# Performance work log

Measured on AMD Instinct MI355X. Metric: run time of the kernel, lower is better.

The kernel has to match this reference:

```python
import jax, jax.numpy as jnp
import numpy as np

B, V = 256, 128000

def setup_inputs() -> dict:
    key = jax.random.key(0)
    k1, k2, k3 = jax.random.split(key, 3)
    logits = jax.random.normal(k1, (B, V), dtype=jnp.float32)
    temperatures = jax.random.uniform(k2, (B,), dtype=jnp.float32)
    top_ps = jax.random.uniform(k3, (B,), dtype=jnp.float32)
    return {"logits": logits, "temperatures": temperatures, "top_ps": top_ps}

def reference(logits, temperatures, top_ps):
    logits = logits.astype(jnp.float32)
    greedy_tokens = jnp.argmax(logits, axis=-1)
    t = temperatures[:, None]
    greedy_mask = t <= 1e-10                       # [B, 1]
    safe_t = jnp.maximum(t, 1e-5)
    probs = jax.nn.softmax(logits / safe_t, axis=-1)  # [B, V]
    # descending sort of probs with indices
    order = jnp.argsort(-probs, axis=-1)           # [B, V]
    sorted_probs = jnp.take_along_axis(probs, order, axis=-1)
    cum = jnp.cumsum(sorted_probs, axis=-1)
    mask = cum > top_ps[:, None]
    mask = mask.at[:, 0].set(False)                # always keep top-1
    sorted_probs = jnp.where(mask, 0.0, sorted_probs)
    # scatter the masked probs back to original vocab positions
    rows = jnp.arange(B)[:, None]
    probs = jnp.zeros_like(probs).at[rows, order].set(sorted_probs)
    probs = probs / jnp.sum(probs, axis=-1, keepdims=True)
    # Gumbel-max style sampling: argmax(probs / Exp(1) noise)
    noise = jax.random.exponential(jax.random.key(1), probs.shape, dtype=jnp.float32)
    noise = jnp.maximum(noise, 1e-10)
    sample_tokens = jnp.argmax(probs / noise, axis=-1)
    return jnp.where(greedy_mask[:, 0], greedy_tokens, sample_tokens)
```

## Files before the change

kernel.cpp:

```cpp
#include <hip/hip_runtime.h>
#include <stdint.h>

typedef unsigned long long u64;
typedef uint32_t u32;

#define BB 256
#define VV 128000
#define NV4 (VV / 4)
#define SLICES 16
#define SL4 (NV4 / SLICES)
#define NBUCK 4096
#define CAP 2048
#define QSCALE 1.099511627776e12f
#define QINV   (1.0 / 1099511627776.0)

#define OFF_SMAX 0
#define OFF_SARG (16*1024)
#define OFF_WWIN (32*1024)
#define OFF_PAR  (64*1024)
#define OFF_CNT  (72*1024)
#define OFF_HIST (80*1024)
#define OFF_LIST (OFF_HIST + (size_t)BB*NBUCK*8)
#define WS_TOTAL (OFF_LIST + (size_t)BB*CAP*8)

struct RowPar { int bstar; float thr; double M; double cutZ; };

#if defined(__has_builtin)
# if __has_builtin(__builtin_amdgcn_sched_barrier)
#  define SCHED_FENCE() __builtin_amdgcn_sched_barrier(0)
# endif
#endif
#ifndef SCHED_FENCE
# define SCHED_FENCE() asm volatile("" ::: "memory")
#endif

__device__ __forceinline__ u32 rotl32(u32 v, u32 r) { return (v << r) | (v >> (32u - r)); }

__device__ __forceinline__ u32 threefry_bits(u32 j) {
    const u32 ks0 = 0u, ks1 = 1u, ks2 = 0x1BD11BDBu;
    u32 x0 = ks0, x1 = j + ks1;
    x0 += x1; x1 = rotl32(x1, 13); x1 ^= x0;
    x0 += x1; x1 = rotl32(x1, 15); x1 ^= x0;
    x0 += x1; x1 = rotl32(x1, 26); x1 ^= x0;
    x0 += x1; x1 = rotl32(x1, 6);  x1 ^= x0;
    x0 += ks1; x1 += ks2 + 1u;
    x0 += x1; x1 = rotl32(x1, 17); x1 ^= x0;
    x0 += x1; x1 = rotl32(x1, 29); x1 ^= x0;
    x0 += x1; x1 = rotl32(x1, 16); x1 ^= x0;
    x0 += x1; x1 = rotl32(x1, 24); x1 ^= x0;
    x0 += ks2; x1 += ks0 + 2u;
    x0 += x1; x1 = rotl32(x1, 13); x1 ^= x0;
    x0 += x1; x1 = rotl32(x1, 15); x1 ^= x0;
    x0 += x1; x1 = rotl32(x1, 26); x1 ^= x0;
    x0 += x1; x1 = rotl32(x1, 6);  x1 ^= x0;
    x0 += ks0; x1 += ks1 + 3u;
    x0 += x1; x1 = rotl32(x1, 17); x1 ^= x0;
    x0 += x1; x1 = rotl32(x1, 29); x1 ^= x0;
    x0 += x1; x1 = rotl32(x1, 16); x1 ^= x0;
    x0 += x1; x1 = rotl32(x1, 24); x1 ^= x0;
    x0 += ks1; x1 += ks2 + 4u;
    x0 += x1; x1 = rotl32(x1, 13); x1 ^= x0;
    x0 += x1; x1 = rotl32(x1, 15); x1 ^= x0;
    x0 += x1; x1 = rotl32(x1, 26); x1 ^= x0;
    x0 += x1; x1 = rotl32(x1, 6);  x1 ^= x0;
    x0 += ks2; x1 += ks0 + 5u;
    return x0 ^ x1;
}

__device__ __forceinline__ float q_of(float x, float invT, float xm) {
    return __expf(fmaf(x, invT, -xm));
}

__device__ __forceinline__ float noise_of(u32 j) {
    u32 bits = threefry_bits(j);
    float u = __uint_as_float((bits >> 9) | 0x3F800000u) - 1.0f;
    return fmaxf(-log1pf(-u), 1e-10f);
}

__device__ __forceinline__ void noise2_of(u32 ja, u32 jb, float& na, float& nb) {
    const u32 ks0 = 0u, ks1 = 1u, ks2 = 0x1BD11BDBu;
    u32 a0 = ks0, a1 = ja + ks1;
    u32 b0 = ks0, b1 = jb + ks1;
#define TF2_RND(r) a0 += a1; a1 = rotl32(a1, r); a1 ^= a0; \
                   b0 += b1; b1 = rotl32(b1, r); b1 ^= b0;
    TF2_RND(13) TF2_RND(15) TF2_RND(26) TF2_RND(6)
    a0 += ks1; a1 += ks2 + 1u;  b0 += ks1; b1 += ks2 + 1u;
    TF2_RND(17) TF2_RND(29) TF2_RND(16) TF2_RND(24)
    a0 += ks2; a1 += ks0 + 2u;  b0 += ks2; b1 += ks0 + 2u;
    TF2_RND(13) TF2_RND(15) TF2_RND(26) TF2_RND(6)
    a0 += ks0; a1 += ks1 + 3u;  b0 += ks0; b1 += ks1 + 3u;
    TF2_RND(17) TF2_RND(29) TF2_RND(16) TF2_RND(24)
    a0 += ks1; a1 += ks2 + 4u;  b0 += ks1; b1 += ks2 + 4u;
    TF2_RND(13) TF2_RND(15) TF2_RND(26) TF2_RND(6)
    a0 += ks2; a1 += ks0 + 5u;  b0 += ks2; b1 += ks0 + 5u;
#undef TF2_RND
    u32 xa = a0 ^ a1, xb = b0 ^ b1;
    float ua = __uint_as_float((xa >> 9) | 0x3F800000u) - 1.0f;
    float ub = __uint_as_float((xb >> 9) | 0x3F800000u) - 1.0f;
    na = fmaxf(-log1pf(-ua), 1e-10f);
    nb = fmaxf(-log1pf(-ub), 1e-10f);
}

extern "C" __global__ void __launch_bounds__(256, 1)
k1_stats(const float* __restrict__ logits, float* __restrict__ smax,
         int* __restrict__ sarg, u64* __restrict__ Whist, int* __restrict__ Wcnt) {
    int blk = blockIdx.x, r = blk >> 4, s = blk & 15;
    int tid = threadIdx.x, lane = tid & 63, wid = tid >> 6;
    __shared__ float sf[4]; __shared__ int si[4];
    Whist[(size_t)r * NBUCK + s * 256 + tid] = 0ULL;
    if (s == 0 && tid == 0) Wcnt[r] = 0;
    const float4* L4 = (const float4*)(logits + (size_t)r * VV);
    int i0 = s * SL4 + tid;
    bool h7 = tid < (SL4 - 7 * 256);
    float4 b0 = L4[i0],          b1 = L4[i0 + 256],  b2 = L4[i0 + 512];
    float4 b3 = L4[i0 + 768],    b4 = L4[i0 + 1024], b5 = L4[i0 + 1280];
    float4 b6 = L4[i0 + 1536],   b7 = L4[h7 ? i0 + 1792 : i0];
    SCHED_FENCE();
    float m = -3.402823466e38f; int mi = 0x7FFFFFFF;
    auto upd = [&](float4 a, int iv) {
        float m4 = fmaxf(fmaxf(a.x, a.y), fmaxf(a.z, a.w));
        if (m4 > m) {
            int base = iv * 4;
            if      (a.x == m4) mi = base;
            else if (a.y == m4) mi = base + 1;
            else if (a.z == m4) mi = base + 2;
            else                mi = base + 3;
            m = m4;
        }
    };
    upd(b0, i0);        upd(b1, i0 + 256);  upd(b2, i0 + 512);  upd(b3, i0 + 768);
    upd(b4, i0 + 1024); upd(b5, i0 + 1280); upd(b6, i0 + 1536);
    if (h7) upd(b7, i0 + 1792);
    for (int off = 32; off; off >>= 1) {
        float ov = __shfl_down(m, off); int oi = __shfl_down(mi, off);
        if (ov > m || (ov == m && oi < mi)) { m = ov; mi = oi; }
    }
    if (lane == 0) { sf[wid] = m; si[wid] = mi; }
    __syncthreads();
    if (tid == 0) {
        for (int w = 1; w < 4; w++) {
            float ov = sf[w]; int oi = si[w];
            if (ov > m || (ov == m && oi < mi)) { m = ov; mi = oi; }
        }
        smax[blk] = m; sarg[blk] = mi;
    }
}

extern "C" __global__ void __launch_bounds__(256, 1)
k2_hist(const float* __restrict__ logits, const float* __restrict__ smax,
        const float* __restrict__ temps, u64* __restrict__ Whist) {
    __shared__ u64 lh[NBUCK];
    int blk = blockIdx.x, r = blk >> 4, s = blk & 15, tid = threadIdx.x;
    for (int i = tid; i < NBUCK; i += 256) lh[i] = 0ULL;
    float T = fmaxf(temps[r], 1e-5f), invT = 1.0f / T;
    float rm = -3.402823466e38f;
    for (int j = 0; j < 16; j++) rm = fmaxf(rm, smax[r * 16 + j]);
    float xm = rm * invT;
    __syncthreads();
    const float4* L4 = (const float4*)(logits + (size_t)r * VV);
    int i0 = s * SL4 + tid;
    bool h7 = tid < (SL4 - 7 * 256);
    float4 b0 = L4[i0],          b1 = L4[i0 + 256],  b2 = L4[i0 + 512];
    float4 b3 = L4[i0 + 768],    b4 = L4[i0 + 1024], b5 = L4[i0 + 1280];
    float4 b6 = L4[i0 + 1536],   b7 = L4[h7 ? i0 + 1792 : i0];
    SCHED_FENCE();
    auto proc = [&](float4 x) {
        float xs[4] = {x.x, x.y, x.z, x.w};
        #pragma unroll
        for (int k = 0; k < 4; k++) {
            float t = fmaf(xs[k], invT, -xm);
            if (t < -27.75f) continue;
            float q = __expf(t);
            u32 pb = __float_as_uint(q);
            if (pb) atomicAdd(&lh[pb >> 18], (u64)(q * QSCALE));
        }
    };
    proc(b0); proc(b1); proc(b2); proc(b3); proc(b4); proc(b5); proc(b6);
    if (h7) proc(b7);
    __syncthreads();
    u64* gh = Whist + (size_t)r * NBUCK;
    for (int i = tid; i < NBUCK; i += 256) {
        u64 v = lh[i];
        if (v) atomicAdd(&gh[i], v);
    }
}

extern "C" __global__ void __launch_bounds__(1024)
k3_cut(const u64* __restrict__ Whist, const float* __restrict__ topps,
       RowPar* __restrict__ par) {
    int r = blockIdx.x, tid = threadIdx.x, lane = tid & 63, wid = tid >> 6;
    __shared__ double wtot[16];
    __shared__ double sh_cutZ; __shared__ int sh_b; __shared__ double sh_M;
    const u64* gh = Whist + (size_t)r * NBUCK;
    double h0 = (double)gh[4 * tid]     * QINV;
    double h1 = (double)gh[4 * tid + 1] * QINV;
    double h2 = (double)gh[4 * tid + 2] * QINV;
    double h3 = (double)gh[4 * tid + 3] * QINV;
    double s3 = h3, s2 = s3 + h2, s1 = s2 + h1, s0 = s1 + h0;
    double incl = s0;
    for (int off = 1; off < 64; off <<= 1) {
        double u = __shfl_down(incl, off);
        if (lane + off < 64) incl += u;
    }
    double excl = __shfl_down(incl, 1); if (lane == 63) excl = 0.0;
    if (lane == 0) wtot[wid] = incl;
    if (tid == 0) { sh_b = -1; sh_M = 0.0; }
    __syncthreads();
    double cw = 0.0;
    for (int w = wid + 1; w < 16; w++) cw += wtot[w];
    double carry = excl + cw;
    if (tid == 0) sh_cutZ = (double)topps[r] * (s0 + carry);
    __syncthreads();
    double cutZ = sh_cutZ;
    double S0 = s0 + carry, S1 = s1 + carry, S2 = s2 + carry, S3 = s3 + carry;
    if (S0 > cutZ && S1 <= cutZ)    { sh_b = 4 * tid;     sh_M = S1; }
    if (S1 > cutZ && S2 <= cutZ)    { sh_b = 4 * tid + 1; sh_M = S2; }
    if (S2 > cutZ && S3 <= cutZ)    { sh_b = 4 * tid + 2; sh_M = S3; }
    if (S3 > cutZ && carry <= cutZ) { sh_b = 4 * tid + 3; sh_M = carry; }
    __syncthreads();
    if (tid == 0) {
        float thr = -3.402823466e38f;
        if (sh_b > 0) {
            float qlo = __uint_as_float((u32)sh_b << 18);
            if (qlo >= 1.17549435e-38f) thr = logf(qlo) - 1e-3f;
        }
        RowPar p; p.bstar = sh_b; p.thr = thr; p.M = sh_M; p.cutZ = cutZ;
        par[r] = p;
    }
}

extern "C" __global__ void __launch_bounds__(256, 1)
k4_race(const float* __restrict__ logits, const float* __restrict__ smax,
        const float* __restrict__ temps, const RowPar* __restrict__ par,
        int* __restrict__ Wcnt, u64* __restrict__ Wlist, u64* __restrict__ Wwin) {
    int blk = blockIdx.x, r = blk >> 4, s = blk & 15;
    int tid = threadIdx.x, lane = tid & 63, wid = tid >> 6;
    __shared__ u64 seg[2][4][257];
    __shared__ int qn[2][4];
    __shared__ u64 wred[4];
    float T = fmaxf(temps[r], 1e-5f), invT = 1.0f / T;
    float rm = -3.402823466e38f;
    for (int j = 0; j < 16; j++) rm = fmaxf(rm, smax[r * 16 + j]);
    float xm = rm * invT;
    int bstar = par[r].bstar;
    float thr = par[r].thr;
    const float4* L4 = (const float4*)(logits + (size_t)r * VV);
    u32 jbase = (u32)r * (u32)VV;
    u64 pk = 0ULL;
    const u64 lanelt = (1ULL << lane) - 1ULL;
    const int dsg = tid & 3, idxb = tid >> 2;
    int i0 = s * SL4 + tid;
    bool h7 = tid < (SL4 - 7 * 256);
    float4 b0 = L4[i0],          b1 = L4[i0 + 256],  b2 = L4[i0 + 512];
    float4 b3 = L4[i0 + 768],    b4 = L4[i0 + 1024], b5 = L4[i0 + 1280];
    float4 b6 = L4[i0 + 1536],   b7 = L4[h7 ? i0 + 1792 : i0];
    SCHED_FENCE();

    auto kfilter = [&](int ph, float4 v, int off, bool valid) {
        float t0 = fmaf(v.x, invT, -xm), t1 = fmaf(v.y, invT, -xm);
        float t2 = fmaf(v.z, invT, -xm), t3 = fmaf(v.w, invT, -xm);
        int base = (i0 + off) * 4;
        bool p0 = valid && (t0 >= thr), p1 = valid && (t1 >= thr);
        bool p2 = valid && (t2 >= thr), p3 = valid && (t3 >= thr);
        u64 m0 = __ballot(p0), m1 = __ballot(p1);
        u64 m2 = __ballot(p2), m3 = __ballot(p3);
        int c0 = __popcll(m0), c01 = c0 + __popcll(m1), c012 = c01 + __popcll(m2);
        u64* sg = seg[ph][wid];
        if (p0) sg[       __popcll(m0 & lanelt)] = ((u64)__float_as_uint(t0) << 32) | (u32)(base + 0);
        if (p1) sg[c0   + __popcll(m1 & lanelt)] = ((u64)__float_as_uint(t1) << 32) | (u32)(base + 1);
        if (p2) sg[c01  + __popcll(m2 & lanelt)] = ((u64)__float_as_uint(t2) << 32) | (u32)(base + 2);
        if (p3) sg[c012 + __popcll(m3 & lanelt)] = ((u64)__float_as_uint(t3) << 32) | (u32)(base + 3);
        if (lane == 0) qn[ph][wid] = c012 + __popcll(m3);
    };

    auto kproc2 = [&](u64 ea, u64 eb, bool va, bool vb) {
        float ta = __uint_as_float((u32)(ea >> 32));
        float tb = __uint_as_float((u32)(eb >> 32));
        u32 dva = (u32)ea, dvb = (u32)eb;
        float qa = __expf(ta), qb = __expf(tb);
        u32 pba = __float_as_uint(qa), pbb = __float_as_uint(qb);
        int bba = (int)(pba >> 18), bbb = (int)(pbb >> 18);
        bool ra = va && pba && (bba > bstar);
        bool rb = vb && pbb && (bbb > bstar);
        if (ra || rb) {
            float nza, nzb;
            noise2_of(jbase + dva, jbase + dvb, nza, nzb);
            if (ra) {
                float sc = __fdividef(qa, nza);
                u64 ee = ((u64)__float_as_uint(sc) << 32) | (u64)(~dva);
                if (ee > pk) pk = ee;
            }
            if (rb) {
                float sc = __fdividef(qb, nzb);
                u64 ee = ((u64)__float_as_uint(sc) << 32) | (u64)(~dvb);
                if (ee > pk) pk = ee;
            }
        }
        if (va && pba && bba == bstar) {
            int pos = atomicAdd(&Wcnt[r], 1);
            if (pos < CAP)
                Wlist[(size_t)r * CAP + pos] = ((u64)pba << 32) | (u64)(~dva);
        }
        if (vb && pbb && bbb == bstar) {
            int pos = atomicAdd(&Wcnt[r], 1);
            if (pos < CAP)
                Wlist[(size_t)r * CAP + pos] = ((u64)pbb << 32) | (u64)(~dvb);
        }
    };
    auto kdense = [&](int ph) {
        int cnt = qn[ph][dsg];
        const u64* sg = seg[ph][dsg];
        u64 e0 = sg[idxb], e1 = sg[idxb + 64], e2 = sg[idxb + 128], e3 = sg[idxb + 192];
        bool v0 = idxb < cnt, v1 = idxb + 64 < cnt;
        bool v2 = idxb + 128 < cnt, v3 = idxb + 192 < cnt;
        if (v0 | v1) kproc2(e0, e1, v0, v1);
        if (v2 | v3) kproc2(e2, e3, v2, v3);
    };

    kfilter(0, b0, 0, true);
    __syncthreads();
    kfilter(1, b1, 256, true);   kdense(0);
    __syncthreads();
    kfilter(0, b2, 512, true);   kdense(1);
    __syncthreads();
    kfilter(1, b3, 768, true);   kdense(0);
    __syncthreads();
    kfilter(0, b4, 1024, true);  kdense(1);
    __syncthreads();
    kfilter(1, b5, 1280, true);  kdense(0);
    __syncthreads();
    kfilter(0, b6, 1536, true);  kdense(1);
    __syncthreads();
    kfilter(1, b7, 1792, h7);    kdense(0);
    __syncthreads();
    kdense(1);

    for (int off = 32; off; off >>= 1) { u64 o = __shfl_down(pk, off); if (o > pk) pk = o; }
    if (lane == 0) wred[wid] = pk;
    __syncthreads();
    if (tid == 0) {
        for (int w = 1; w < 4; w++) if (wred[w] > pk) pk = wred[w];
        Wwin[blk] = pk;
    }
}

extern "C" __global__ void __launch_bounds__(1024)
k5_final(const float* __restrict__ smax, const int* __restrict__ sarg,
         const float* __restrict__ temps, const float* __restrict__ topps,
         const RowPar* __restrict__ par, const int* __restrict__ Wcnt,
         const u64* __restrict__ Wlist, const u64* __restrict__ Wwin,
         int* __restrict__ out) {
    int r = blockIdx.x, tid = threadIdx.x, lane = tid & 63, wid = tid >> 6;
    __shared__ u64 sb[CAP];
    __shared__ double wtot[16];
    __shared__ u64 wred[16];
    __shared__ int sh_js, sh_n, sh_gidx; __shared__ float sh_rm;
    RowPar p = par[r];
    if (tid == 0) {
        float rm = -3.402823466e38f; int gi = 0x7FFFFFFF;
        for (int j = 0; j < 16; j++) {
            float v = smax[r * 16 + j];
            if (v > rm) { rm = v; gi = sarg[r * 16 + j]; }
        }
        sh_rm = rm; sh_gidx = gi;
        int n = Wcnt[r]; if (n > CAP) n = CAP; sh_n = n;
        sh_js = 0x7FFFFFFF;
    }
    __syncthreads();
    int n = sh_n;
    int npad = 4; while (npad < n) npad <<= 1;
    const u64* lst = Wlist + (size_t)r * CAP;
    for (int i = tid; i < npad; i += 1024) sb[i] = (i < n) ? lst[i] : 0ULL;
    __syncthreads();
    for (int k = 2; k <= npad; k <<= 1) {
        for (int j = k >> 1; j > 0; j >>= 1) {
            for (int i = tid; i < npad; i += 1024) {
                int q2 = i ^ j;
                if (q2 > i) {
                    u64 a = sb[i], b = sb[q2];
                    bool desc = ((i & k) == 0);
                    if (desc ? (a < b) : (a > b)) { sb[i] = b; sb[q2] = a; }
                }
            }
            __syncthreads();
        }
    }
    int t2 = tid * 2;
    double f0 = 0.0, f1 = 0.0;
    if (t2 < npad) {
        f0 = (double)__uint_as_float((u32)(sb[t2] >> 32));
        f1 = (double)__uint_as_float((u32)(sb[t2 + 1] >> 32));
    }
    double c0 = f0, c1 = c0 + f1;
    double incl = c1;
    for (int off = 1; off < 64; off <<= 1) {
        double u = __shfl_up(incl, off);
        if (lane >= off) incl += u;
    }
    double excl = __shfl_up(incl, 1); if (lane == 0) excl = 0.0;
    double wt = __shfl(incl, 63);
    if (lane == 0) wtot[wid] = wt;
    __syncthreads();
    double cw = 0.0;
    for (int w = 0; w < wid; w++) cw += wtot[w];
    double cr = cw + excl;
    if (t2 < npad) {
        bool m0 = (p.M + (cr + c0)) > p.cutZ;
        bool m1 = (p.M + (cr + c1)) > p.cutZ;
        int cand = m0 ? t2 : m1 ? (t2 + 1) : 0x7FFFFFFF;
        if (cand != 0x7FFFFFFF) atomicMin(&sh_js, cand);
    }
    __syncthreads();
    float Traw = temps[r];
    if (tid == 0) {
        int js = sh_js; if (js > n) js = n;
        float T = fmaxf(Traw, 1e-5f), invT = 1.0f / T, xm = sh_rm * invT;
        int btop = (int)(__float_as_uint(q_of(sh_rm, invT, xm)) >> 18);
        if (js == 0 && p.bstar == btop) js = 1;
        sh_js = js;
    }
    __syncthreads();
    int js = sh_js;
    u32 jbase = (u32)r * (u32)VV;
    u64 pk = 0ULL;
    for (int i = tid; i < js; i += 1024) {
        u64 key = sb[i];
        float qq = __uint_as_float((u32)(key >> 32));
        u32 v = ~(u32)key;
        float nz = noise_of(jbase + v);
        float sc = __fdividef(qq, nz);
        u64 e = ((u64)__float_as_uint(sc) << 32) | (u64)(~v);
        if (e > pk) pk = e;
    }
    if (tid < 16) { u64 w = Wwin[r * 16 + tid]; if (w > pk) pk = w; }
    for (int off = 32; off; off >>= 1) { u64 o = __shfl_down(pk, off); if (o > pk) pk = o; }
    if (lane == 0) wred[wid] = pk;
    __syncthreads();
    if (tid == 0) {
        for (int w = 1; w < 16; w++) if (wred[w] > pk) pk = wred[w];
        int bi = (int)(~(u32)pk);
        out[r] = (Traw <= 1e-10f) ? sh_gidx : bi;
    }
}

extern "C" __global__ void __launch_bounds__(1024, 1)
sampler_fallback(const float* __restrict__ logits, const float* __restrict__ temps,
                 const float* __restrict__ topps, int* __restrict__ out)
{
    const int row = blockIdx.x;
    const int tid = threadIdx.x;
    const int lane = tid & 63;
    const int wid = tid >> 6;
    const float* L = logits + (size_t)row * VV;
    const float4* L4 = (const float4*)L;
    __shared__ __align__(16) unsigned char SMEM[32768];
    float* hist = (float*)SMEM;
    u64* sortbuf = (u64*)SMEM;
    __shared__ double wtot[16];
    __shared__ float wredf[16];
    __shared__ int wredi[16];
    __shared__ float sh_lmax;
    __shared__ int sh_gidx;
    __shared__ double sh_cutZ;
    __shared__ double sh_M;
    __shared__ int sh_bstar;
    __shared__ int sh_ng;
    __shared__ int sh_jstar;
    const float Traw = temps[row];
    const float T = fmaxf(Traw, 1e-5f);
    const float invT = 1.0f / T;
    const float tp = topps[row];
    float lmax = -3.402823466e38f; int lidx = 0x7FFFFFFF;
    for (int iv = tid; iv < NV4; iv += 1024) {
        float4 x = L4[iv];
        float m4 = fmaxf(fmaxf(x.x, x.y), fmaxf(x.z, x.w));
        if (m4 > lmax) {
            int base = iv * 4;
            if      (x.x == m4) lidx = base;
            else if (x.y == m4) lidx = base + 1;
            else if (x.z == m4) lidx = base + 2;
            else                lidx = base + 3;
            lmax = m4;
        }
    }
    for (int off = 32; off > 0; off >>= 1) {
        float ov = __shfl_down(lmax, off);
        int   oi = __shfl_down(lidx, off);
        if (ov > lmax || (ov == lmax && oi < lidx)) { lmax = ov; lidx = oi; }
    }
    if (lane == 0) { wredf[wid] = lmax; wredi[wid] = lidx; }
    for (int i = tid; i < NBUCK; i += 1024) hist[i] = 0.0f;
    __syncthreads();
    if (wid == 0) {
        float v = (lane < 16) ? wredf[lane] : -3.402823466e38f;
        int   i = (lane < 16) ? wredi[lane] : 0x7FFFFFFF;
        for (int off = 32; off > 0; off >>= 1) {
            float ov = __shfl_down(v, off);
            int   oi = __shfl_down(i, off);
            if (ov > v || (ov == v && oi < i)) { v = ov; i = oi; }
        }
        if (lane == 0) { sh_lmax = v; sh_gidx = i; }
    }
    __syncthreads();
    const float xm = sh_lmax * invT;
    const int gidx = sh_gidx;
    const int btop = (int)(__float_as_uint(q_of(sh_lmax, invT, xm)) >> 18);
    for (int iv = tid; iv < NV4; iv += 1024) {
        float4 x = L4[iv];
        float q0 = q_of(x.x, invT, xm), q1 = q_of(x.y, invT, xm);
        float q2 = q_of(x.z, invT, xm), q3 = q_of(x.w, invT, xm);
        u32 b0 = __float_as_uint(q0), b1 = __float_as_uint(q1);
        u32 b2 = __float_as_uint(q2), b3 = __float_as_uint(q3);
        if (b0) atomicAdd(&hist[b0 >> 18], q0);
        if (b1) atomicAdd(&hist[b1 >> 18], q1);
        if (b2) atomicAdd(&hist[b2 >> 18], q2);
        if (b3) atomicAdd(&hist[b3 >> 18], q3);
    }
    __syncthreads();
    float h0 = hist[4 * tid], h1 = hist[4 * tid + 1],
          h2 = hist[4 * tid + 2], h3 = hist[4 * tid + 3];
    double s3 = (double)h3, s2 = s3 + (double)h2, s1 = s2 + (double)h1, s0 = s1 + (double)h0;
    double incl = s0;
    for (int off = 1; off < 64; off <<= 1) {
        double u = __shfl_down(incl, off);
        if (lane + off < 64) incl += u;
    }
    double excl = __shfl_down(incl, 1);
    if (lane == 63) excl = 0.0;
    if (lane == 0) wtot[wid] = incl;
    __syncthreads();
    double cw = 0.0;
    for (int w = wid + 1; w < 16; w++) cw += wtot[w];
    const double carry = excl + cw;
    if (tid == 0) {
        sh_cutZ = (double)tp * (s0 + carry);
        sh_bstar = -1; sh_M = 0.0; sh_ng = 0; sh_jstar = 0x7FFFFFFF;
    }
    __syncthreads();
    const double cutZ = sh_cutZ;
    {
        double S0 = s0 + carry, S1 = s1 + carry, S2 = s2 + carry, S3 = s3 + carry;
        if (S0 > cutZ && S1 <= cutZ)    { sh_bstar = 4 * tid;     sh_M = S1; }
        if (S1 > cutZ && S2 <= cutZ)    { sh_bstar = 4 * tid + 1; sh_M = S2; }
        if (S2 > cutZ && S3 <= cutZ)    { sh_bstar = 4 * tid + 2; sh_M = S3; }
        if (S3 > cutZ && carry <= cutZ) { sh_bstar = 4 * tid + 3; sh_M = carry; }
    }
    __syncthreads();
    const int bstar = sh_bstar;
    const double M = sh_M;
    float bs = -1.0f; int bi = 0x7FFFFFFF;
    const u32 jbase = (u32)row * (u32)VV;
    for (int iv = tid; iv < NV4; iv += 1024) {
        float4 x = L4[iv];
        float qs[4] = {q_of(x.x, invT, xm), q_of(x.y, invT, xm),
                       q_of(x.z, invT, xm), q_of(x.w, invT, xm)};
        int base = iv * 4;
        #pragma unroll
        for (int k = 0; k < 4; k++) {
            u32 pb = __float_as_uint(qs[k]);
            if (pb == 0u) continue;
            int b = (int)(pb >> 18);
            if (b > bstar) {
                int v = base + k;
                float nz = noise_of(jbase + (u32)v);
                float sc = __fdividef(qs[k], nz);
                if (sc > bs || (sc == bs && v < bi)) { bs = sc; bi = v; }
            } else if (b == bstar) {
                int pos = atomicAdd(&sh_ng, 1);
                if (pos < 4096)
                    sortbuf[pos] = ((u64)pb << 32) | (u32)(~(u32)(base + k));
            }
        }
    }
    __syncthreads();
    if (bstar >= 0) {
        int n = sh_ng; if (n > 4096) n = 4096;
        int npad = 4; while (npad < n) npad <<= 1;
        for (int i = tid; i < npad; i += 1024) if (i >= n) sortbuf[i] = 0ULL;
        __syncthreads();
        for (int k = 2; k <= npad; k <<= 1) {
            for (int j = k >> 1; j > 0; j >>= 1) {
                for (int i = tid; i < npad; i += 1024) {
                    int pidx = i ^ j;
                    if (pidx > i) {
                        u64 a = sortbuf[i], b2 = sortbuf[pidx];
                        bool desc = ((i & k) == 0);
                        if (desc ? (a < b2) : (a > b2)) { sortbuf[i] = b2; sortbuf[pidx] = a; }
                    }
                }
                __syncthreads();
            }
        }
        double f0 = 0.0, f1 = 0.0, f2 = 0.0, f3 = 0.0;
        int t4 = tid * 4;
        if (t4 < npad) {
            f0 = (double)__uint_as_float((u32)(sortbuf[t4]     >> 32));
            f1 = (double)__uint_as_float((u32)(sortbuf[t4 + 1] >> 32));
            f2 = (double)__uint_as_float((u32)(sortbuf[t4 + 2] >> 32));
            f3 = (double)__uint_as_float((u32)(sortbuf[t4 + 3] >> 32));
        }
        double c0 = f0, c1 = c0 + f1, c2 = c1 + f2, c3 = c2 + f3;
        double incl2 = c3;
        for (int off = 1; off < 64; off <<= 1) {
            double u = __shfl_up(incl2, off);
            if (lane >= off) incl2 += u;
        }
        double excl2 = __shfl_up(incl2, 1);
        if (lane == 0) excl2 = 0.0;
        double wt = __shfl(incl2, 63);
        if (lane == 0) wtot[wid] = wt;
        __syncthreads();
        double cw2 = 0.0;
        for (int w = 0; w < wid; w++) cw2 += wtot[w];
        double cr = cw2 + excl2;
        if (t4 < npad) {
            bool m0 = (M + (cr + c0)) > cutZ;
            bool m1 = (M + (cr + c1)) > cutZ;
            bool m2 = (M + (cr + c2)) > cutZ;
            bool m3 = (M + (cr + c3)) > cutZ;
            int cand = m0 ? t4 : m1 ? (t4 + 1) : m2 ? (t4 + 2) : m3 ? (t4 + 3) : 0x7FFFFFFF;
            if (cand != 0x7FFFFFFF) atomicMin(&sh_jstar, cand);
        }
        __syncthreads();
        int jstar = sh_jstar; if (jstar > n) jstar = n;
        if (jstar == 0 && bstar == btop) jstar = 1;
        for (int i = tid; i < jstar; i += 1024) {
            u64 key = sortbuf[i];
            float qq = __uint_as_float((u32)(key >> 32));
            int v = (int)(~(u32)key);
            float nz = noise_of(jbase + (u32)v);
            float sc = __fdividef(qq, nz);
            if (sc > bs || (sc == bs && v < bi)) { bs = sc; bi = v; }
        }
    }
    for (int off = 32; off > 0; off >>= 1) {
        float ov = __shfl_down(bs, off);
        int   oi = __shfl_down(bi, off);
        if (ov > bs || (ov == bs && oi < bi)) { bs = ov; bi = oi; }
    }
    if (lane == 0) { wredf[wid] = bs; wredi[wid] = bi; }
    __syncthreads();
    if (tid == 0) {
        float v = wredf[0]; int i = wredi[0];
        for (int w = 1; w < 16; w++) {
            float ov = wredf[w]; int oi = wredi[w];
            if (ov > v || (ov == v && oi < i)) { v = ov; i = oi; }
        }
        out[row] = (Traw <= 1e-10f) ? gidx : i;
    }
}

extern "C" void kernel_launch(void* const* d_in, const int* in_sizes, int n_in,
                              void* d_out, int out_size, void* d_ws, size_t ws_size,
                              hipStream_t stream) {
    const float* logits = (const float*)d_in[0];
    const float* temps = (const float*)d_in[1];
    const float* topps = (const float*)d_in[2];
    int* out = (int*)d_out;
    (void)in_sizes; (void)n_in; (void)out_size;

    if (ws_size >= WS_TOTAL) {
        char* ws = (char*)d_ws;
        float* smax  = (float*)(ws + OFF_SMAX);
        int*   sarg  = (int*)(ws + OFF_SARG);
        u64*   wwin  = (u64*)(ws + OFF_WWIN);
        RowPar* par  = (RowPar*)(ws + OFF_PAR);
        int*   wcnt  = (int*)(ws + OFF_CNT);
        u64*   whist = (u64*)(ws + OFF_HIST);
        u64*   wlist = (u64*)(ws + OFF_LIST);
        k1_stats<<<BB * SLICES, 256, 0, stream>>>(logits, smax, sarg, whist, wcnt);
        k2_hist<<<BB * SLICES, 256, 0, stream>>>(logits, smax, temps, whist);
        k3_cut<<<BB, 1024, 0, stream>>>(whist, topps, par);
        k4_race<<<BB * SLICES, 256, 0, stream>>>(logits, smax, temps, par, wcnt, wlist, wwin);
        k5_final<<<BB, 1024, 0, stream>>>(smax, sarg, temps, topps, par, wcnt, wlist, wwin, out);
    } else {
        sampler_fallback<<<BB, 1024, 0, stream>>>(logits, temps, topps, out);
    }
}
```

Baseline: 348.6 us.

## Merge two k4 slices per 512-thread block and aggregate bucket-list atomics per wave

k4_race now launches 8 blocks of 512 threads per row instead of 16 blocks of 256, with each block covering two vocab slices. The dense phase spreads work over 8 wave segments. Per-element atomicAdd on the row counter is replaced by a wave-level ballot, one atomic per wave and a shuffle of the base index, which cuts atomic contention. As a side effect, the kproc2 calls are no longer skipped when both entries are invalid, so the per-wave ballots run uniformly. k5 reads 8 per-block winners instead of 16.

```diff
diff --git a/kernel.cpp b/kernel.cpp
--- a/kernel.cpp
+++ b/kernel.cpp
@@ -229,15 +229,17 @@
     }
 }
 
-extern "C" __global__ void __launch_bounds__(256, 1)
+extern "C" __global__ void __launch_bounds__(512, 1)
 k4_race(const float* __restrict__ logits, const float* __restrict__ smax,
         const float* __restrict__ temps, const RowPar* __restrict__ par,
         int* __restrict__ Wcnt, u64* __restrict__ Wlist, u64* __restrict__ Wwin) {
-    int blk = blockIdx.x, r = blk >> 4, s = blk & 15;
+    int blk = blockIdx.x, r = blk >> 3, sp = blk & 7;
     int tid = threadIdx.x, lane = tid & 63, wid = tid >> 6;
-    __shared__ u64 seg[2][4][257];
-    __shared__ int qn[2][4];
-    __shared__ u64 wred[4];
+    int tloc = tid & 255;
+    int s = sp * 2 + (tid >> 8);
+    __shared__ u64 seg[2][8][257];
+    __shared__ int qn[2][8];
+    __shared__ u64 wred[8];
     float T = fmaxf(temps[r], 1e-5f), invT = 1.0f / T;
     float rm = -3.402823466e38f;
     for (int j = 0; j < 16; j++) rm = fmaxf(rm, smax[r * 16 + j]);
@@ -248,9 +250,9 @@
     u32 jbase = (u32)r * (u32)VV;
     u64 pk = 0ULL;
     const u64 lanelt = (1ULL << lane) - 1ULL;
-    const int dsg = tid & 3, idxb = tid >> 2;
-    int i0 = s * SL4 + tid;
-    bool h7 = tid < (SL4 - 7 * 256);
+    const int dsg = tid & 7, idxb = tid >> 3;
+    int i0 = s * SL4 + tloc;
+    bool h7 = tloc < (SL4 - 7 * 256);
     float4 b0 = L4[i0],          b1 = L4[i0 + 256],  b2 = L4[i0 + 512];
     float4 b3 = L4[i0 + 768],    b4 = L4[i0 + 1024], b5 = L4[i0 + 1280];
     float4 b6 = L4[i0 + 1536],   b7 = L4[h7 ? i0 + 1792 : i0];
@@ -273,6 +275,20 @@
         if (lane == 0) qn[ph][wid] = c012 + __popcll(m3);
     };
 
+    auto emit_bstar = [&](bool isb, u32 pb, u32 dv) {
+        u64 bm = __ballot(isb);
+        if (bm) {
+            int cnt = __popcll(bm);
+            int base = 0;
+            if (lane == 0) base = atomicAdd(&Wcnt[r], cnt);
+            base = __shfl(base, 0);
+            if (isb) {
+                int pos = base + __popcll(bm & lanelt);
+                if (pos < CAP)
+                    Wlist[(size_t)r * CAP + pos] = ((u64)pb << 32) | (u64)(~dv);
+            }
+        }
+    };
     auto kproc2 = [&](u64 ea, u64 eb, bool va, bool vb) {
         float ta = __uint_as_float((u32)(ea >> 32));
         float tb = __uint_as_float((u32)(eb >> 32));
@@ -296,16 +312,8 @@
                 if (ee > pk) pk = ee;
             }
         }
-        if (va && pba && bba == bstar) {
-            int pos = atomicAdd(&Wcnt[r], 1);
-            if (pos < CAP)
-                Wlist[(size_t)r * CAP + pos] = ((u64)pba << 32) | (u64)(~dva);
-        }
-        if (vb && pbb && bbb == bstar) {
-            int pos = atomicAdd(&Wcnt[r], 1);
-            if (pos < CAP)
-                Wlist[(size_t)r * CAP + pos] = ((u64)pbb << 32) | (u64)(~dvb);
-        }
+        emit_bstar(va && pba && (bba == bstar), pba, dva);
+        emit_bstar(vb && pbb && (bbb == bstar), pbb, dvb);
     };
     auto kdense = [&](int ph) {
         int cnt = qn[ph][dsg];
@@ -313,8 +321,8 @@
         u64 e0 = sg[idxb], e1 = sg[idxb + 64], e2 = sg[idxb + 128], e3 = sg[idxb + 192];
         bool v0 = idxb < cnt, v1 = idxb + 64 < cnt;
         bool v2 = idxb + 128 < cnt, v3 = idxb + 192 < cnt;
-        if (v0 | v1) kproc2(e0, e1, v0, v1);
-        if (v2 | v3) kproc2(e2, e3, v2, v3);
+        kproc2(e0, e1, v0, v1);
+        kproc2(e2, e3, v2, v3);
     };
 
     kfilter(0, b0, 0, true);
@@ -339,7 +347,7 @@
     if (lane == 0) wred[wid] = pk;
     __syncthreads();
     if (tid == 0) {
-        for (int w = 1; w < 4; w++) if (wred[w] > pk) pk = wred[w];
+        for (int w = 1; w < 8; w++) if (wred[w] > pk) pk = wred[w];
         Wwin[blk] = pk;
     }
 }
@@ -432,7 +440,7 @@
         u64 e = ((u64)__float_as_uint(sc) << 32) | (u64)(~v);
         if (e > pk) pk = e;
     }
-    if (tid < 16) { u64 w = Wwin[r * 16 + tid]; if (w > pk) pk = w; }
+    if (tid < 8) { u64 w = Wwin[r * 8 + tid]; if (w > pk) pk = w; }
     for (int off = 32; off; off >>= 1) { u64 o = __shfl_down(pk, off); if (o > pk) pk = o; }
     if (lane == 0) wred[wid] = pk;
     __syncthreads();
@@ -671,7 +679,7 @@
         k1_stats<<<BB * SLICES, 256, 0, stream>>>(logits, smax, sarg, whist, wcnt);
         k2_hist<<<BB * SLICES, 256, 0, stream>>>(logits, smax, temps, whist);
         k3_cut<<<BB, 1024, 0, stream>>>(whist, topps, par);
-        k4_race<<<BB * SLICES, 256, 0, stream>>>(logits, smax, temps, par, wcnt, wlist, wwin);
+        k4_race<<<BB * 8, 512, 0, stream>>>(logits, smax, temps, par, wcnt, wlist, wwin);
         k5_final<<<BB, 1024, 0, stream>>>(smax, sarg, temps, topps, par, wcnt, wlist, wwin, out);
     } else {
         sampler_fallback<<<BB, 1024, 0, stream>>>(logits, temps, topps, out);
```

After: 354.2 us. About the same (+1.6%).

## Schedule rows by descending temperature and simplify race-kernel shared segment indexing

Applied to the files above, without the earlier changes.

Adds a small bitonic-sort kernel that orders rows by descending temperature. The histogram and race kernels use that permutation to map blocks to rows, so rows with heavier work (high temperature, many survivors of the filter) are dispatched first and there is less tail imbalance. The race kernel's dense phase now has each thread read one entry from each of the four wave segments, instead of the padded strided layout, and the row-stride padding is removed. The cost is an extra launch and a per-block permutation load, and the new shared-memory layout may bring back bank conflicts.

```diff
diff --git a/kernel.cpp b/kernel.cpp
--- a/kernel.cpp
+++ b/kernel.cpp
@@ -19,6 +19,7 @@
 #define OFF_WWIN (32*1024)
 #define OFF_PAR  (64*1024)
 #define OFF_CNT  (72*1024)
+#define OFF_PERM (76*1024)
 #define OFF_HIST (80*1024)
 #define OFF_LIST (OFF_HIST + (size_t)BB*NBUCK*8)
 #define WS_TOTAL (OFF_LIST + (size_t)BB*CAP*8)
@@ -102,6 +103,27 @@
 }
 
 extern "C" __global__ void __launch_bounds__(256, 1)
+k0_perm(const float* __restrict__ temps, int* __restrict__ perm) {
+    __shared__ u64 sk[256];
+    int tid = threadIdx.x;
+    float t = temps[tid];
+    sk[tid] = ((u64)__float_as_uint(t) << 32) | (u32)tid;
+    __syncthreads();
+    for (int k = 2; k <= 256; k <<= 1) {
+        for (int j = k >> 1; j > 0; j >>= 1) {
+            int q2 = tid ^ j;
+            if (q2 > tid) {
+                u64 a = sk[tid], b = sk[q2];
+                bool desc = ((tid & k) == 0);
+                if (desc ? (a < b) : (a > b)) { sk[tid] = b; sk[q2] = a; }
+            }
+            __syncthreads();
+        }
+    }
+    perm[tid] = (int)(u32)(sk[tid] & 0xFFFFFFFFu);
+}
+
+extern "C" __global__ void __launch_bounds__(256, 1)
 k1_stats(const float* __restrict__ logits, float* __restrict__ smax,
          int* __restrict__ sarg, u64* __restrict__ Whist, int* __restrict__ Wcnt) {
     int blk = blockIdx.x, r = blk >> 4, s = blk & 15;
@@ -148,9 +170,10 @@
 
 extern "C" __global__ void __launch_bounds__(256, 1)
 k2_hist(const float* __restrict__ logits, const float* __restrict__ smax,
-        const float* __restrict__ temps, u64* __restrict__ Whist) {
+        const float* __restrict__ temps, u64* __restrict__ Whist,
+        const int* __restrict__ perm) {
     __shared__ u64 lh[NBUCK];
-    int blk = blockIdx.x, r = blk >> 4, s = blk & 15, tid = threadIdx.x;
+    int blk = blockIdx.x, r = perm[blk >> 4], s = blk & 15, tid = threadIdx.x;
     for (int i = tid; i < NBUCK; i += 256) lh[i] = 0ULL;
     float T = fmaxf(temps[r], 1e-5f), invT = 1.0f / T;
     float rm = -3.402823466e38f;
@@ -232,10 +255,11 @@
 extern "C" __global__ void __launch_bounds__(256, 1)
 k4_race(const float* __restrict__ logits, const float* __restrict__ smax,
         const float* __restrict__ temps, const RowPar* __restrict__ par,
-        int* __restrict__ Wcnt, u64* __restrict__ Wlist, u64* __restrict__ Wwin) {
-    int blk = blockIdx.x, r = blk >> 4, s = blk & 15;
+        int* __restrict__ Wcnt, u64* __restrict__ Wlist, u64* __restrict__ Wwin,
+        const int* __restrict__ perm) {
+    int blk = blockIdx.x, r = perm[blk >> 4], s = blk & 15;
     int tid = threadIdx.x, lane = tid & 63, wid = tid >> 6;
-    __shared__ u64 seg[2][4][257];
+    __shared__ u64 seg[2][4][256];
     __shared__ int qn[2][4];
     __shared__ u64 wred[4];
     float T = fmaxf(temps[r], 1e-5f), invT = 1.0f / T;
@@ -248,7 +272,6 @@
     u32 jbase = (u32)r * (u32)VV;
     u64 pk = 0ULL;
     const u64 lanelt = (1ULL << lane) - 1ULL;
-    const int dsg = tid & 3, idxb = tid >> 2;
     int i0 = s * SL4 + tid;
     bool h7 = tid < (SL4 - 7 * 256);
     float4 b0 = L4[i0],          b1 = L4[i0 + 256],  b2 = L4[i0 + 512];
@@ -308,11 +331,10 @@
         }
     };
     auto kdense = [&](int ph) {
-        int cnt = qn[ph][dsg];
-        const u64* sg = seg[ph][dsg];
-        u64 e0 = sg[idxb], e1 = sg[idxb + 64], e2 = sg[idxb + 128], e3 = sg[idxb + 192];
-        bool v0 = idxb < cnt, v1 = idxb + 64 < cnt;
-        bool v2 = idxb + 128 < cnt, v3 = idxb + 192 < cnt;
+        int c0 = qn[ph][0], c1 = qn[ph][1], c2 = qn[ph][2], c3 = qn[ph][3];
+        u64 e0 = seg[ph][0][tid], e1 = seg[ph][1][tid];
+        u64 e2 = seg[ph][2][tid], e3 = seg[ph][3][tid];
+        bool v0 = tid < c0, v1 = tid < c1, v2 = tid < c2, v3 = tid < c3;
         if (v0 | v1) kproc2(e0, e1, v0, v1);
         if (v2 | v3) kproc2(e2, e3, v2, v3);
     };
@@ -340,7 +362,7 @@
     __syncthreads();
     if (tid == 0) {
         for (int w = 1; w < 4; w++) if (wred[w] > pk) pk = wred[w];
-        Wwin[blk] = pk;
+        Wwin[r * 16 + s] = pk;
     }
 }
 
@@ -666,12 +688,14 @@
         u64*   wwin  = (u64*)(ws + OFF_WWIN);
         RowPar* par  = (RowPar*)(ws + OFF_PAR);
         int*   wcnt  = (int*)(ws + OFF_CNT);
+        int*   perm  = (int*)(ws + OFF_PERM);
         u64*   whist = (u64*)(ws + OFF_HIST);
         u64*   wlist = (u64*)(ws + OFF_LIST);
+        k0_perm<<<1, 256, 0, stream>>>(temps, perm);
         k1_stats<<<BB * SLICES, 256, 0, stream>>>(logits, smax, sarg, whist, wcnt);
-        k2_hist<<<BB * SLICES, 256, 0, stream>>>(logits, smax, temps, whist);
+        k2_hist<<<BB * SLICES, 256, 0, stream>>>(logits, smax, temps, whist, perm);
         k3_cut<<<BB, 1024, 0, stream>>>(whist, topps, par);
-        k4_race<<<BB * SLICES, 256, 0, stream>>>(logits, smax, temps, par, wcnt, wlist, wwin);
+        k4_race<<<BB * SLICES, 256, 0, stream>>>(logits, smax, temps, par, wcnt, wlist, wwin, perm);
         k5_final<<<BB, 1024, 0, stream>>>(smax, sarg, temps, topps, par, wcnt, wlist, wwin, out);
     } else {
         sampler_fallback<<<BB, 1024, 0, stream>>>(logits, temps, topps, out);
```

New measurement: 410.0 us. +17.6%, slower.
